# Performance work log

Hardware: AMD Instinct MI355X
Metric: run time of the kernel (lower is better)

Reference implementation:

```python
import jax, jax.numpy as jnp
import numpy as np

D = 128          # size_in
SIGN = 4         # Linear_v5 default sign
CONST = 0.618    # additive constant after sigmoid


def setup_inputs() -> dict:
    key = jax.random.key(0)
    k = jax.random.split(key, 6)
    N = 8192
    return {
        "t": jnp.zeros((1,), jnp.float32),  # unused time argument
        "input_": jax.random.normal(k[0], (N, 2 * D), jnp.float32),
        "W1": jax.random.normal(k[1], (2 * D, D), jnp.float32) * 0.05,
        "b1": jax.random.normal(k[2], (2 * D,), jnp.float32) * 0.05,
        "W2": jax.random.normal(k[3], (D, 2 * D), jnp.float32) * 0.05,
        "b2": jax.random.normal(k[4], (D,), jnp.float32) * 0.05,
    }


def _g_and_jac(x, W1, b1, W2, b2):
    """g(x) = sign * (sigmoid(W2 relu(W1 x + b1) + b2) + 0.618) and its
    per-sample Jacobian dg_i/dx_j, computed analytically (same math as
    torch.autograd.functional.jacobian of the sum over batch, permuted)."""
    sign_vec = jnp.where(jnp.arange(D) < SIGN, -1.0, 1.0).astype(x.dtype)
    z1 = x @ W1.T + b1                      # [N, 2D]
    h = jax.nn.relu(z1)
    s = jax.nn.sigmoid(h @ W2.T + b2)       # [N, D]
    g = (s + CONST) * sign_vec              # [N, D]
    mask = (z1 > 0).astype(x.dtype)         # relu'(z1), [N, 2D]
    coef = sign_vec * s * (1.0 - s)         # sigmoid' with sign flip, [N, D]
    # jac[n,i,j] = coef[n,i] * sum_k W2[i,k] * mask[n,k] * W1[k,j]
    jac = jnp.einsum('ni,ik,nk,kj->nij', coef, W2, mask, W1)  # [N, D, D]
    return g, jac


def reference(t, input_, W1, b1, W2, b2):
    x = input_[:, :D]
    v = input_[:, D:]
    g, jac = _g_and_jac(x, W1, b1, W2, b2)
    g_inv = 1.0 / g                              # [N, D]
    case1 = -jac * g_inv[:, None, :]             # [N, i, j] * g_inv[:, j]
    case2 = jac * g_inv[:, :, None]              # [N, i, j] * g_inv[:, i]
    # dv_vec[n,i,j] = v_i v_j (never materialized; folded into einsums)
    t1 = jnp.einsum('ni,nij->nj', v * v, case1)          # sum_i v_i^2 case1[n,i,j]
    t2 = jnp.einsum('nj,ni,nji->nj', v, v, case2)        # einsum('hji,hji->hj')
    t3 = jnp.einsum('ni,nj,nji->nj', v, v, case2)        # einsum('hij,hji->hj')
    dv = t1 + t2 + t3
    return jnp.hstack([v, dv])                            # [N, 2D]
```

## Files before the change

### kernel.cpp

```cpp
#include <hip/hip_runtime.h>

#define D_  128
#define K2_ 256
#define BM  32

typedef short bf16x8 __attribute__((ext_vector_type(8)));
typedef float f32x4  __attribute__((ext_vector_type(4)));

__device__ __forceinline__ unsigned short f2bf(float f) {
  unsigned int u = __float_as_uint(f);
  u += 0x7fffu + ((u >> 16) & 1u);
  return (unsigned short)(u >> 16);
}
__device__ __forceinline__ float bf2f(unsigned short s) {
  return __uint_as_float(((unsigned int)s) << 16);
}

__global__ __launch_bounds__(256) void fused_jvp_kernel(
    const float* __restrict__ input_,
    const float* __restrict__ W1, const float* __restrict__ b1,
    const float* __restrict__ W2, const float* __restrict__ b2,
    float* __restrict__ out)
{
  __shared__ __align__(16) unsigned short xb [BM * D_];
  __shared__ __align__(16) unsigned short xlb[BM * D_];
  __shared__ __align__(16) unsigned short vb [BM * D_];
  __shared__ __align__(16) unsigned short ub [BM * D_];
  __shared__ __align__(16) unsigned short hb [BM * K2_];
  __shared__ __align__(16) unsigned short m2b[BM * K2_];
  __shared__ __align__(16) unsigned short rb [BM * K2_];

  const int tid  = threadIdx.x;
  const int lane = tid & 63;
  const int wv   = tid >> 6;
  const int l15  = lane & 15;
  const int lg   = lane >> 4;
  const long rowbase = (long)blockIdx.x * BM;

  #pragma unroll
  for (int it = 0; it < 8; ++it) {
    int flat4 = it * 256 + tid;
    int row   = flat4 >> 6;
    int col   = (flat4 & 63) * 4;
    const float4 val = *(const float4*)(input_ + (rowbase + row) * 256 + col);
    ushort4 hq;
    hq.x = f2bf(val.x); hq.y = f2bf(val.y); hq.z = f2bf(val.z); hq.w = f2bf(val.w);
    if (col < D_) {
      ushort4 lq;
      lq.x = f2bf(val.x - bf2f(hq.x));
      lq.y = f2bf(val.y - bf2f(hq.y));
      lq.z = f2bf(val.z - bf2f(hq.z));
      lq.w = f2bf(val.w - bf2f(hq.w));
      int idx = (row * D_ + col) ^ ((row & 7) << 3);
      *(ushort4*)(&xb[idx])  = hq;
      *(ushort4*)(&xlb[idx]) = lq;
    } else {
      int c = col - D_;
      int idx = (row * D_ + c) ^ ((row & 7) << 3);
      *(ushort4*)(&vb[idx]) = hq;
      *(float4*)(out + (rowbase + row) * 256 + c) = val;
    }
  }
  __syncthreads();

  auto load_afrag = [&](const unsigned short* tile, int S, int rbase, int kbase) -> bf16x8 {
    int row = rbase + l15;
    int idx = (row * S + kbase + lg * 8) ^ ((row & 7) << 3);
    return *(const bf16x8*)(&tile[idx]);
  };
  auto load_bfrag_row = [&](const float* Wp, int Kd, int colbase, int kbase) -> bf16x8 {
    const float* p = Wp + (size_t)(colbase + l15) * Kd + kbase + lg * 8;
    float4 f0 = *(const float4*)p;
    float4 f1 = *(const float4*)(p + 4);
    bf16x8 r;
    r[0]=(short)f2bf(f0.x); r[1]=(short)f2bf(f0.y); r[2]=(short)f2bf(f0.z); r[3]=(short)f2bf(f0.w);
    r[4]=(short)f2bf(f1.x); r[5]=(short)f2bf(f1.y); r[6]=(short)f2bf(f1.z); r[7]=(short)f2bf(f1.w);
    return r;
  };
  auto load_bfrag_row_pair = [&](const float* Wp, int Kd, int colbase, int kbase,
                                 bf16x8* hi, bf16x8* lo) {
    const float* p = Wp + (size_t)(colbase + l15) * Kd + kbase + lg * 8;
    float4 f0 = *(const float4*)p;
    float4 f1 = *(const float4*)(p + 4);
    float fv[8] = {f0.x, f0.y, f0.z, f0.w, f1.x, f1.y, f1.z, f1.w};
    #pragma unroll
    for (int e = 0; e < 8; ++e) {
      unsigned short h = f2bf(fv[e]);
      (*hi)[e] = (short)h;
      (*lo)[e] = (short)f2bf(fv[e] - bf2f(h));
    }
  };
  auto load_bfrag_T = [&](const float* Wp, int Fd, int colbase, int kbase) -> bf16x8 {
    const float* p = Wp + (size_t)(kbase + lg * 8) * Fd + colbase + l15;
    bf16x8 r;
    #pragma unroll
    for (int e = 0; e < 8; ++e) r[e] = (short)f2bf(p[e * Fd]);
    return r;
  };

  f32x4 accz[2][4] = {};
  f32x4 accw[2][4] = {};
  for (int kk = 0; kk < D_; kk += 32) {
    bf16x8 bwh[4], bwl[4];
    #pragma unroll
    for (int nt = 0; nt < 4; ++nt)
      load_bfrag_row_pair(W1, D_, wv * 64 + nt * 16, kk, &bwh[nt], &bwl[nt]);
    #pragma unroll
    for (int mt = 0; mt < 2; ++mt) {
      bf16x8 axh = load_afrag(xb,  D_, mt * 16, kk);
      bf16x8 axl = load_afrag(xlb, D_, mt * 16, kk);
      bf16x8 av  = load_afrag(vb,  D_, mt * 16, kk);
      #pragma unroll
      for (int nt = 0; nt < 4; ++nt) {
        accz[mt][nt] = __builtin_amdgcn_mfma_f32_16x16x32_bf16(axh, bwh[nt], accz[mt][nt], 0, 0, 0);
        accz[mt][nt] = __builtin_amdgcn_mfma_f32_16x16x32_bf16(axh, bwl[nt], accz[mt][nt], 0, 0, 0);
        accz[mt][nt] = __builtin_amdgcn_mfma_f32_16x16x32_bf16(axl, bwh[nt], accz[mt][nt], 0, 0, 0);
        accw[mt][nt] = __builtin_amdgcn_mfma_f32_16x16x32_bf16(av,  bwh[nt], accw[mt][nt], 0, 0, 0);
      }
    }
  }
  #pragma unroll
  for (int mt = 0; mt < 2; ++mt)
  #pragma unroll
  for (int nt = 0; nt < 4; ++nt) {
    int cg = wv * 64 + nt * 16 + l15;
    float bias = b1[cg];
    #pragma unroll
    for (int q = 0; q < 4; ++q) {
      int rg = mt * 16 + lg * 4 + q;
      float z = accz[mt][nt][q] + bias;
      if (__builtin_expect(fabsf(z) < 1e-4f, 0)) {
        const float* xr  = input_ + (rowbase + rg) * 256;
        const float* w1r = W1 + (size_t)cg * D_;
        double zd = (double)bias;
        for (int k = 0; k < D_; ++k) zd += (double)xr[k] * (double)w1r[k];
        z = (float)zd;
      }
      float hv = z > 0.f ? z : 0.f;
      float mw = z > 0.f ? accw[mt][nt][q] : 0.f;
      int idx = (rg * K2_ + cg) ^ ((rg & 7) << 3);
      hb[idx]  = f2bf(hv);
      m2b[idx] = f2bf(mw);
    }
  }
  __syncthreads();

  f32x4 accs[2][2] = {};
  f32x4 accy[2][2] = {};
  for (int kk = 0; kk < K2_; kk += 32) {
    bf16x8 bw[2];
    #pragma unroll
    for (int nt = 0; nt < 2; ++nt) bw[nt] = load_bfrag_row(W2, K2_, wv * 32 + nt * 16, kk);
    #pragma unroll
    for (int mt = 0; mt < 2; ++mt) {
      bf16x8 ah = load_afrag(hb,  K2_, mt * 16, kk);
      bf16x8 am = load_afrag(m2b, K2_, mt * 16, kk);
      #pragma unroll
      for (int nt = 0; nt < 2; ++nt) {
        accs[mt][nt] = __builtin_amdgcn_mfma_f32_16x16x32_bf16(ah, bw[nt], accs[mt][nt], 0, 0, 0);
        accy[mt][nt] = __builtin_amdgcn_mfma_f32_16x16x32_bf16(am, bw[nt], accy[mt][nt], 0, 0, 0);
      }
    }
  }
  float coefr[2][2][4], ginvr[2][2][4];
  #pragma unroll
  for (int mt = 0; mt < 2; ++mt)
  #pragma unroll
  for (int nt = 0; nt < 2; ++nt) {
    int cg = wv * 32 + nt * 16 + l15;
    float bias = b2[cg];
    float sgn  = (cg < 4) ? -1.f : 1.f;
    #pragma unroll
    for (int q = 0; q < 4; ++q) {
      int rg = mt * 16 + lg * 4 + q;
      float sv = 1.f / (1.f + __expf(-(accs[mt][nt][q] + bias)));
      float cf = sgn * sv * (1.f - sv);
      float gi = 1.f / ((sv + 0.618f) * sgn);
      coefr[mt][nt][q] = cf;
      ginvr[mt][nt][q] = gi;
      float vvf = input_[(rowbase + rg) * 256 + 128 + cg];
      int idxd = (rg * D_ + cg) ^ ((rg & 7) << 3);
      ub[idxd] = f2bf(vvf * vvf * cf);
    }
  }
  __syncthreads();

  f32x4 accp[2][4] = {};
  for (int kk = 0; kk < D_; kk += 32) {
    bf16x8 bw[4];
    #pragma unroll
    for (int nt = 0; nt < 4; ++nt) bw[nt] = load_bfrag_T(W2, K2_, wv * 64 + nt * 16, kk);
    #pragma unroll
    for (int mt = 0; mt < 2; ++mt) {
      bf16x8 au = load_afrag(ub, D_, mt * 16, kk);
      #pragma unroll
      for (int nt = 0; nt < 4; ++nt)
        accp[mt][nt] = __builtin_amdgcn_mfma_f32_16x16x32_bf16(au, bw[nt], accp[mt][nt], 0, 0, 0);
    }
  }
  #pragma unroll
  for (int mt = 0; mt < 2; ++mt)
  #pragma unroll
  for (int nt = 0; nt < 4; ++nt) {
    int cg = wv * 64 + nt * 16 + l15;
    #pragma unroll
    for (int q = 0; q < 4; ++q) {
      int rg = mt * 16 + lg * 4 + q;
      int idx = (rg * K2_ + cg) ^ ((rg & 7) << 3);
      rb[idx] = (hb[idx] != 0) ? f2bf(accp[mt][nt][q]) : (unsigned short)0;
    }
  }
  __syncthreads();

  f32x4 acct[2][2] = {};
  for (int kk = 0; kk < K2_; kk += 32) {
    bf16x8 bw[2];
    #pragma unroll
    for (int nt = 0; nt < 2; ++nt) bw[nt] = load_bfrag_T(W1, D_, wv * 32 + nt * 16, kk);
    #pragma unroll
    for (int mt = 0; mt < 2; ++mt) {
      bf16x8 ar = load_afrag(rb, K2_, mt * 16, kk);
      #pragma unroll
      for (int nt = 0; nt < 2; ++nt)
        acct[mt][nt] = __builtin_amdgcn_mfma_f32_16x16x32_bf16(ar, bw[nt], acct[mt][nt], 0, 0, 0);
    }
  }
  #pragma unroll
  for (int mt = 0; mt < 2; ++mt)
  #pragma unroll
  for (int nt = 0; nt < 2; ++nt) {
    int cg = wv * 32 + nt * 16 + l15;
    #pragma unroll
    for (int q = 0; q < 4; ++q) {
      int rg = mt * 16 + lg * 4 + q;
      float vvf = input_[(rowbase + rg) * 256 + 128 + cg];
      float gi  = ginvr[mt][nt][q];
      float dv  = -gi * acct[mt][nt][q]
                + 2.f * vvf * gi * coefr[mt][nt][q] * accy[mt][nt][q];
      out[(rowbase + rg) * 256 + 128 + cg] = dv;
    }
  }
}

extern "C" void kernel_launch(void* const* d_in, const int* in_sizes, int n_in,
                              void* d_out, int out_size, void* d_ws, size_t ws_size,
                              hipStream_t stream) {
  const float* input_ = (const float*)d_in[1];
  const float* W1     = (const float*)d_in[2];
  const float* b1     = (const float*)d_in[3];
  const float* W2     = (const float*)d_in[4];
  const float* b2     = (const float*)d_in[5];
  float* out = (float*)d_out;
  int N = in_sizes[1] / (2 * D_);
  fused_jvp_kernel<<<dim3(N / BM), dim3(256), 0, stream>>>(input_, W1, b1, W2, b2, out);
}
```

Before: 30.23 us.

## Prepack weights into MFMA fragment layout and halve row tile with LDS aliasing

Adds a prep kernel that converts W1 and W2, including the transposed copies and the W1 lo-split, to bf16 laid out in MFMA B-fragment order in workspace. Each B fragment then becomes one contiguous 16-byte load instead of per-block strided fp32 loads and conversions. The row tile shrinks from 32 to 16 to double the block count, and shared buffers are aliased to cut LDS use and raise occupancy. The cost is an extra kernel launch each call and more total weight reads from global memory or cache per row processed.

Measured after the change: 34.32 us. 13.5% more time.

```diff
diff --git a/kernel.cpp b/kernel.cpp
--- a/kernel.cpp
+++ b/kernel.cpp
@@ -2,7 +2,7 @@
 
 #define D_  128
 #define K2_ 256
-#define BM  32
+#define BM  16
 
 typedef short bf16x8 __attribute__((ext_vector_type(8)));
 typedef float f32x4  __attribute__((ext_vector_type(4)));
@@ -16,19 +16,51 @@
   return __uint_as_float(((unsigned int)s) << 16);
 }
 
+__global__ __launch_bounds__(256) void prep_pack(
+    const float* __restrict__ W1, const float* __restrict__ W2,
+    unsigned short* __restrict__ ws)
+{
+  int idx = blockIdx.x * 256 + threadIdx.x;
+  int p   = idx >> 15;
+  int r   = idx & 32767;
+  int e   = r & 7;
+  int l   = (r >> 3) & 63;
+  int blk = r >> 9;
+  int sh  = (p == 2 || p == 4) ? 3 : 2;
+  int k32 = blk & ((1 << sh) - 1);
+  int c16 = blk >> sh;
+  int c = c16 * 16 + (l & 15);
+  int k = k32 * 32 + (l >> 4) * 8 + e;
+  float v;
+  if (p <= 1)      v = W1[c * 128 + k];
+  else if (p == 2) v = W2[c * 256 + k];
+  else if (p == 3) v = W2[k * 256 + c];
+  else             v = W1[k * 128 + c];
+  unsigned short h = f2bf(v);
+  ws[idx] = (p == 1) ? f2bf(v - bf2f(h)) : h;
+}
+
 __global__ __launch_bounds__(256) void fused_jvp_kernel(
     const float* __restrict__ input_,
     const float* __restrict__ W1, const float* __restrict__ b1,
-    const float* __restrict__ W2, const float* __restrict__ b2,
+    const float* __restrict__ b2,
+    const unsigned short* __restrict__ wp,
     float* __restrict__ out)
 {
-  __shared__ __align__(16) unsigned short xb [BM * D_];
-  __shared__ __align__(16) unsigned short xlb[BM * D_];
-  __shared__ __align__(16) unsigned short vb [BM * D_];
-  __shared__ __align__(16) unsigned short ub [BM * D_];
-  __shared__ __align__(16) unsigned short hb [BM * K2_];
-  __shared__ __align__(16) unsigned short m2b[BM * K2_];
-  __shared__ __align__(16) unsigned short rb [BM * K2_];
+  __shared__ __align__(16) unsigned short sh[14336];
+  unsigned short* xb  = sh;
+  unsigned short* xlb = sh + 2048;
+  unsigned short* vb  = sh + 4096;
+  unsigned short* hb  = sh + 6144;
+  unsigned short* m2b = sh + 10240;
+  unsigned short* ub  = sh;
+  unsigned short* rb  = sh + 10240;
+
+  const unsigned short* p0 = wp;
+  const unsigned short* p1 = wp + 32768;
+  const unsigned short* p2 = wp + 65536;
+  const unsigned short* p3 = wp + 98304;
+  const unsigned short* p4 = wp + 131072;
 
   const int tid  = threadIdx.x;
   const int lane = tid & 63;
@@ -38,7 +70,7 @@
   const long rowbase = (long)blockIdx.x * BM;
 
   #pragma unroll
-  for (int it = 0; it < 8; ++it) {
+  for (int it = 0; it < 4; ++it) {
     int flat4 = it * 256 + tid;
     int row   = flat4 >> 6;
     int col   = (flat4 & 63) * 4;
@@ -63,72 +95,41 @@
   }
   __syncthreads();
 
-  auto load_afrag = [&](const unsigned short* tile, int S, int rbase, int kbase) -> bf16x8 {
-    int row = rbase + l15;
+  auto load_afrag = [&](const unsigned short* tile, int S, int kbase) -> bf16x8 {
+    int row = l15;
     int idx = (row * S + kbase + lg * 8) ^ ((row & 7) << 3);
     return *(const bf16x8*)(&tile[idx]);
   };
-  auto load_bfrag_row = [&](const float* Wp, int Kd, int colbase, int kbase) -> bf16x8 {
-    const float* p = Wp + (size_t)(colbase + l15) * Kd + kbase + lg * 8;
-    float4 f0 = *(const float4*)p;
-    float4 f1 = *(const float4*)(p + 4);
-    bf16x8 r;
-    r[0]=(short)f2bf(f0.x); r[1]=(short)f2bf(f0.y); r[2]=(short)f2bf(f0.z); r[3]=(short)f2bf(f0.w);
-    r[4]=(short)f2bf(f1.x); r[5]=(short)f2bf(f1.y); r[6]=(short)f2bf(f1.z); r[7]=(short)f2bf(f1.w);
-    return r;
+  auto ldB = [&](const unsigned short* pk, int K32, int c16, int k32) -> bf16x8 {
+    return *(const bf16x8*)(pk + (((c16 * K32 + k32) << 9) + (lane << 3)));
   };
-  auto load_bfrag_row_pair = [&](const float* Wp, int Kd, int colbase, int kbase,
-                                 bf16x8* hi, bf16x8* lo) {
-    const float* p = Wp + (size_t)(colbase + l15) * Kd + kbase + lg * 8;
-    float4 f0 = *(const float4*)p;
-    float4 f1 = *(const float4*)(p + 4);
-    float fv[8] = {f0.x, f0.y, f0.z, f0.w, f1.x, f1.y, f1.z, f1.w};
-    #pragma unroll
-    for (int e = 0; e < 8; ++e) {
-      unsigned short h = f2bf(fv[e]);
-      (*hi)[e] = (short)h;
-      (*lo)[e] = (short)f2bf(fv[e] - bf2f(h));
-    }
-  };
-  auto load_bfrag_T = [&](const float* Wp, int Fd, int colbase, int kbase) -> bf16x8 {
-    const float* p = Wp + (size_t)(kbase + lg * 8) * Fd + colbase + l15;
-    bf16x8 r;
-    #pragma unroll
-    for (int e = 0; e < 8; ++e) r[e] = (short)f2bf(p[e * Fd]);
-    return r;
-  };
-
-  f32x4 accz[2][4] = {};
-  f32x4 accw[2][4] = {};
-  for (int kk = 0; kk < D_; kk += 32) {
-    bf16x8 bwh[4], bwl[4];
-    #pragma unroll
-    for (int nt = 0; nt < 4; ++nt)
-      load_bfrag_row_pair(W1, D_, wv * 64 + nt * 16, kk, &bwh[nt], &bwl[nt]);
-    #pragma unroll
-    for (int mt = 0; mt < 2; ++mt) {
-      bf16x8 axh = load_afrag(xb,  D_, mt * 16, kk);
-      bf16x8 axl = load_afrag(xlb, D_, mt * 16, kk);
-      bf16x8 av  = load_afrag(vb,  D_, mt * 16, kk);
-      #pragma unroll
-      for (int nt = 0; nt < 4; ++nt) {
-        accz[mt][nt] = __builtin_amdgcn_mfma_f32_16x16x32_bf16(axh, bwh[nt], accz[mt][nt], 0, 0, 0);
-        accz[mt][nt] = __builtin_amdgcn_mfma_f32_16x16x32_bf16(axh, bwl[nt], accz[mt][nt], 0, 0, 0);
-        accz[mt][nt] = __builtin_amdgcn_mfma_f32_16x16x32_bf16(axl, bwh[nt], accz[mt][nt], 0, 0, 0);
-        accw[mt][nt] = __builtin_amdgcn_mfma_f32_16x16x32_bf16(av,  bwh[nt], accw[mt][nt], 0, 0, 0);
-      }
-    }
-  }
-  #pragma unroll
-  for (int mt = 0; mt < 2; ++mt)
+
+  f32x4 accz[4] = {};
+  f32x4 accw[4] = {};
+  #pragma unroll
+  for (int k32 = 0; k32 < 4; ++k32) {
+    bf16x8 axh = load_afrag(xb,  D_, k32 * 32);
+    bf16x8 axl = load_afrag(xlb, D_, k32 * 32);
+    bf16x8 av  = load_afrag(vb,  D_, k32 * 32);
+    #pragma unroll
+    for (int nt = 0; nt < 4; ++nt) {
+      int c16 = wv * 4 + nt;
+      bf16x8 bh = ldB(p0, 4, c16, k32);
+      bf16x8 bl = ldB(p1, 4, c16, k32);
+      accz[nt] = __builtin_amdgcn_mfma_f32_16x16x32_bf16(axh, bh, accz[nt], 0, 0, 0);
+      accz[nt] = __builtin_amdgcn_mfma_f32_16x16x32_bf16(axh, bl, accz[nt], 0, 0, 0);
+      accz[nt] = __builtin_amdgcn_mfma_f32_16x16x32_bf16(axl, bh, accz[nt], 0, 0, 0);
+      accw[nt] = __builtin_amdgcn_mfma_f32_16x16x32_bf16(av,  bh, accw[nt], 0, 0, 0);
+    }
+  }
   #pragma unroll
   for (int nt = 0; nt < 4; ++nt) {
     int cg = wv * 64 + nt * 16 + l15;
     float bias = b1[cg];
     #pragma unroll
     for (int q = 0; q < 4; ++q) {
-      int rg = mt * 16 + lg * 4 + q;
-      float z = accz[mt][nt][q] + bias;
+      int rg = lg * 4 + q;
+      float z = accz[nt][q] + bias;
       if (__builtin_expect(fabsf(z) < 1e-4f, 0)) {
         const float* xr  = input_ + (rowbase + rg) * 256;
         const float* w1r = W1 + (size_t)cg * D_;
@@ -137,7 +138,7 @@
         z = (float)zd;
       }
       float hv = z > 0.f ? z : 0.f;
-      float mw = z > 0.f ? accw[mt][nt][q] : 0.f;
+      float mw = z > 0.f ? accw[nt][q] : 0.f;
       int idx = (rg * K2_ + cg) ^ ((rg & 7) << 3);
       hb[idx]  = f2bf(hv);
       m2b[idx] = f2bf(mw);
@@ -145,26 +146,21 @@
   }
   __syncthreads();
 
-  f32x4 accs[2][2] = {};
-  f32x4 accy[2][2] = {};
-  for (int kk = 0; kk < K2_; kk += 32) {
-    bf16x8 bw[2];
-    #pragma unroll
-    for (int nt = 0; nt < 2; ++nt) bw[nt] = load_bfrag_row(W2, K2_, wv * 32 + nt * 16, kk);
-    #pragma unroll
-    for (int mt = 0; mt < 2; ++mt) {
-      bf16x8 ah = load_afrag(hb,  K2_, mt * 16, kk);
-      bf16x8 am = load_afrag(m2b, K2_, mt * 16, kk);
-      #pragma unroll
-      for (int nt = 0; nt < 2; ++nt) {
-        accs[mt][nt] = __builtin_amdgcn_mfma_f32_16x16x32_bf16(ah, bw[nt], accs[mt][nt], 0, 0, 0);
-        accy[mt][nt] = __builtin_amdgcn_mfma_f32_16x16x32_bf16(am, bw[nt], accy[mt][nt], 0, 0, 0);
-      }
-    }
-  }
-  float coefr[2][2][4], ginvr[2][2][4];
-  #pragma unroll
-  for (int mt = 0; mt < 2; ++mt)
+  f32x4 accs[2] = {};
+  f32x4 accy[2] = {};
+  #pragma unroll
+  for (int k32 = 0; k32 < 8; ++k32) {
+    bf16x8 ah = load_afrag(hb,  K2_, k32 * 32);
+    bf16x8 am = load_afrag(m2b, K2_, k32 * 32);
+    #pragma unroll
+    for (int nt = 0; nt < 2; ++nt) {
+      int c16 = wv * 2 + nt;
+      bf16x8 bw = ldB(p2, 8, c16, k32);
+      accs[nt] = __builtin_amdgcn_mfma_f32_16x16x32_bf16(ah, bw, accs[nt], 0, 0, 0);
+      accy[nt] = __builtin_amdgcn_mfma_f32_16x16x32_bf16(am, bw, accy[nt], 0, 0, 0);
+    }
+  }
+  float coefr[2][4], ginvr[2][4];
   #pragma unroll
   for (int nt = 0; nt < 2; ++nt) {
     int cg = wv * 32 + nt * 16 + l15;
@@ -172,12 +168,12 @@
     float sgn  = (cg < 4) ? -1.f : 1.f;
     #pragma unroll
     for (int q = 0; q < 4; ++q) {
-      int rg = mt * 16 + lg * 4 + q;
-      float sv = 1.f / (1.f + __expf(-(accs[mt][nt][q] + bias)));
+      int rg = lg * 4 + q;
+      float sv = 1.f / (1.f + __expf(-(accs[nt][q] + bias)));
       float cf = sgn * sv * (1.f - sv);
       float gi = 1.f / ((sv + 0.618f) * sgn);
-      coefr[mt][nt][q] = cf;
-      ginvr[mt][nt][q] = gi;
+      coefr[nt][q] = cf;
+      ginvr[nt][q] = gi;
       float vvf = input_[(rowbase + rg) * 256 + 128 + cg];
       int idxd = (rg * D_ + cg) ^ ((rg & 7) << 3);
       ub[idxd] = f2bf(vvf * vvf * cf);
@@ -185,58 +181,50 @@
   }
   __syncthreads();
 
-  f32x4 accp[2][4] = {};
-  for (int kk = 0; kk < D_; kk += 32) {
-    bf16x8 bw[4];
-    #pragma unroll
-    for (int nt = 0; nt < 4; ++nt) bw[nt] = load_bfrag_T(W2, K2_, wv * 64 + nt * 16, kk);
-    #pragma unroll
-    for (int mt = 0; mt < 2; ++mt) {
-      bf16x8 au = load_afrag(ub, D_, mt * 16, kk);
-      #pragma unroll
-      for (int nt = 0; nt < 4; ++nt)
-        accp[mt][nt] = __builtin_amdgcn_mfma_f32_16x16x32_bf16(au, bw[nt], accp[mt][nt], 0, 0, 0);
-    }
-  }
-  #pragma unroll
-  for (int mt = 0; mt < 2; ++mt)
+  f32x4 accp[4] = {};
+  #pragma unroll
+  for (int k32 = 0; k32 < 4; ++k32) {
+    bf16x8 au = load_afrag(ub, D_, k32 * 32);
+    #pragma unroll
+    for (int nt = 0; nt < 4; ++nt) {
+      int c16 = wv * 4 + nt;
+      bf16x8 bw = ldB(p3, 4, c16, k32);
+      accp[nt] = __builtin_amdgcn_mfma_f32_16x16x32_bf16(au, bw, accp[nt], 0, 0, 0);
+    }
+  }
   #pragma unroll
   for (int nt = 0; nt < 4; ++nt) {
     int cg = wv * 64 + nt * 16 + l15;
     #pragma unroll
     for (int q = 0; q < 4; ++q) {
-      int rg = mt * 16 + lg * 4 + q;
+      int rg = lg * 4 + q;
       int idx = (rg * K2_ + cg) ^ ((rg & 7) << 3);
-      rb[idx] = (hb[idx] != 0) ? f2bf(accp[mt][nt][q]) : (unsigned short)0;
-    }
-  }
-  __syncthreads();
-
-  f32x4 acct[2][2] = {};
-  for (int kk = 0; kk < K2_; kk += 32) {
-    bf16x8 bw[2];
-    #pragma unroll
-    for (int nt = 0; nt < 2; ++nt) bw[nt] = load_bfrag_T(W1, D_, wv * 32 + nt * 16, kk);
-    #pragma unroll
-    for (int mt = 0; mt < 2; ++mt) {
-      bf16x8 ar = load_afrag(rb, K2_, mt * 16, kk);
-      #pragma unroll
-      for (int nt = 0; nt < 2; ++nt)
-        acct[mt][nt] = __builtin_amdgcn_mfma_f32_16x16x32_bf16(ar, bw[nt], acct[mt][nt], 0, 0, 0);
-    }
-  }
-  #pragma unroll
-  for (int mt = 0; mt < 2; ++mt)
+      rb[idx] = (hb[idx] != 0) ? f2bf(accp[nt][q]) : (unsigned short)0;
+    }
+  }
+  __syncthreads();
+
+  f32x4 acct[2] = {};
+  #pragma unroll
+  for (int k32 = 0; k32 < 8; ++k32) {
+    bf16x8 ar = load_afrag(rb, K2_, k32 * 32);
+    #pragma unroll
+    for (int nt = 0; nt < 2; ++nt) {
+      int c16 = wv * 2 + nt;
+      bf16x8 bw = ldB(p4, 8, c16, k32);
+      acct[nt] = __builtin_amdgcn_mfma_f32_16x16x32_bf16(ar, bw, acct[nt], 0, 0, 0);
+    }
+  }
   #pragma unroll
   for (int nt = 0; nt < 2; ++nt) {
     int cg = wv * 32 + nt * 16 + l15;
     #pragma unroll
     for (int q = 0; q < 4; ++q) {
-      int rg = mt * 16 + lg * 4 + q;
+      int rg = lg * 4 + q;
       float vvf = input_[(rowbase + rg) * 256 + 128 + cg];
-      float gi  = ginvr[mt][nt][q];
-      float dv  = -gi * acct[mt][nt][q]
-                + 2.f * vvf * gi * coefr[mt][nt][q] * accy[mt][nt][q];
+      float gi  = ginvr[nt][q];
+      float dv  = -gi * acct[nt][q]
+                + 2.f * vvf * gi * coefr[nt][q] * accy[nt][q];
       out[(rowbase + rg) * 256 + 128 + cg] = dv;
     }
   }
@@ -251,6 +239,9 @@
   const float* W2     = (const float*)d_in[4];
   const float* b2     = (const float*)d_in[5];
   float* out = (float*)d_out;
+  unsigned short* wpack = (unsigned short*)d_ws;
   int N = in_sizes[1] / (2 * D_);
-  fused_jvp_kernel<<<dim3(N / BM), dim3(256), 0, stream>>>(input_, W1, b1, W2, b2, out);
-}
+
+  prep_pack<<<dim3(640), dim3(256), 0, stream>>>(W1, W2, wpack);
+  fused_jvp_kernel<<<dim3(N / BM), dim3(256), 0, stream>>>(input_, W1, b1, b2, wpack, out);
+}
```
